# Kernel optimization log

Hardware: AMD Instinct MI355X
Metric: run time of the kernel (lower is better)

## Reference

```python
import jax, jax.numpy as jnp
import numpy as np

EPS_NN = 1e-8   # inverse-distance epsilon (PointNet++ three_interpolate)
EPS_BN = 1e-5   # BatchNorm eps


def three_nn_interpolate(points_coords, centers_coords, centers_features):
    # points_coords: [B,3,N], centers_coords: [B,3,M], centers_features: [B,C,M]
    # squared pairwise distances [B,N,M]
    d2 = jnp.sum((points_coords[:, :, :, None] - centers_coords[:, :, None, :]) ** 2, axis=1)
    neg_d, idx = jax.lax.top_k(-d2, 3)            # idx: [B,N,3]
    dist = -neg_d                                  # 3 smallest squared distances
    w = 1.0 / (dist + EPS_NN)
    w = w / jnp.sum(w, axis=-1, keepdims=True)     # [B,N,3]
    # gather center features at the 3 neighbors -> [B,C,N,3]
    f = jnp.take_along_axis(centers_features[:, :, None, :], idx[:, None, :, :], axis=3)
    return jnp.sum(f * w[:, None, :, :], axis=-1)  # [B,C,N]


def conv_bn_relu(x, w, b, gamma, beta):
    # x: [B,Cin,N], w: [Cout,Cin] (1x1 Conv1d), BatchNorm1d (training-mode batch stats)
    y = jnp.einsum('oc,bcn->bon', w, x) + b[None, :, None]
    mean = jnp.mean(y, axis=(0, 2), keepdims=True)
    var = jnp.var(y, axis=(0, 2), keepdims=True)
    y = (y - mean) * jax.lax.rsqrt(var + EPS_BN)
    y = y * gamma[None, :, None] + beta[None, :, None]
    return jax.nn.relu(y)


def setup_inputs() -> dict:
    key = jax.random.key(0)
    ks = jax.random.split(key, 10)
    B, N, M, C, C2 = 8, 8192, 2048, 256, 256
    Cin = C + C2
    O1, O2 = 256, 256
    return {
        'points_coords': jax.random.normal(ks[0], (B, 3, N), dtype=jnp.float32),
        'centers_coords': jax.random.normal(ks[1], (B, 3, M), dtype=jnp.float32),
        'centers_features': jax.random.normal(ks[2], (B, C, M), dtype=jnp.float32),
        'points_features': jax.random.normal(ks[3], (B, C2, N), dtype=jnp.float32),
        'w1': jax.random.normal(ks[4], (O1, Cin), dtype=jnp.float32) * (1.0 / np.sqrt(Cin)),
        'b1': jnp.zeros((O1,), dtype=jnp.float32),
        'gamma1': jnp.ones((O1,), dtype=jnp.float32),
        'beta1': jnp.zeros((O1,), dtype=jnp.float32),
        'w2': jax.random.normal(ks[5], (O2, O1), dtype=jnp.float32) * (1.0 / np.sqrt(O1)),
        'b2': jnp.zeros((O2,), dtype=jnp.float32),
        'gamma2': jnp.ones((O2,), dtype=jnp.float32),
        'beta2': jnp.zeros((O2,), dtype=jnp.float32),
    }


def reference(points_coords, centers_coords, centers_features, points_features,
              w1, b1, gamma1, beta1, w2, b2, gamma2, beta2):
    interp = three_nn_interpolate(points_coords, centers_coords, centers_features)  # [B,C,N]
    x = jnp.concatenate([interp, points_features], axis=1)                          # [B,C+C2,N]
    x = conv_bn_relu(x, w1, b1, gamma1, beta1)
    x = conv_bn_relu(x, w2, b2, gamma2, beta2)
    return (x, points_coords)
```

## Files before the change

kernel.cpp:

```cpp
#include <hip/hip_runtime.h>


#define BB 8
#define NN 8192
#define MM 2048
#define CF 256
#define CP 256

typedef float f4 __attribute__((ext_vector_type(4)));
typedef short s8v __attribute__((ext_vector_type(8)));

union U4 { uint4 u; s8v s; };

#define OFF_IDX    ((size_t)0)
#define OFF_WGT    ((size_t)1 << 20)
#define OFF_INTERP ((size_t)2 << 20)
#define OFF_P1S    (OFF_INTERP + (size_t)BB*CF*NN*4)
#define OFF_P1Q    (OFF_P1S + (size_t)512*256*4)
#define OFF_P2S    (OFF_P1Q + (size_t)512*256*4)
#define OFF_P2Q    (OFF_P2S + (size_t)512*256*4)
#define OFF_PAR1   (OFF_P2Q + (size_t)512*256*4)
#define OFF_PAR2   (OFF_PAR1 + (size_t)256*8)
#define OFF_WP1    (OFF_PAR2 + (size_t)256*8)
#define OFF_WP2    (OFF_WP1 + (size_t)524288)

__device__ __forceinline__ f4 relu4(f4 v) {
    v.x = fmaxf(v.x, 0.f); v.y = fmaxf(v.y, 0.f);
    v.z = fmaxf(v.z, 0.f); v.w = fmaxf(v.w, 0.f);
    return v;
}

__device__ __forceinline__ ushort bfrn(float x) {
    unsigned u = __float_as_uint(x);
    return (ushort)((u + 0x7FFFu + ((u >> 16) & 1u)) >> 16);
}
__device__ __forceinline__ void split1(float v, ushort& h, ushort& lo) {
    h = bfrn(v);
    float hf = __uint_as_float(((unsigned)h) << 16);
    lo = bfrn(v - hf);
}
__device__ __forceinline__ uint4 pack8(const ushort* h) {
    uint4 u;
    u.x = (unsigned)h[0] | ((unsigned)h[1] << 16);
    u.y = (unsigned)h[2] | ((unsigned)h[3] << 16);
    u.z = (unsigned)h[4] | ((unsigned)h[5] << 16);
    u.w = (unsigned)h[6] | ((unsigned)h[7] << 16);
    return u;
}

__global__ void k_wsplit(const float* __restrict__ w1, const float* __restrict__ w2,
                         uint4* __restrict__ wp1, uint4* __restrict__ wp2) {
    int i = blockIdx.x * 256 + threadIdx.x;
    const float* src; uint4* dst; int kt, o, kh, kdim;
    if (i < 16384) { kdim = 512; kt = i >> 10; int r = i & 1023; o = r >> 2; kh = r & 3; src = w1; dst = wp1; }
    else { int j = i - 16384; kdim = 256; kt = j >> 10; int r = j & 1023; o = r >> 2; kh = r & 3; src = w2; dst = wp2; }
    const float* p = src + o * kdim + kt * 32 + kh * 8;
    ushort hh[8], ll[8];
    #pragma unroll
    for (int k = 0; k < 8; ++k) split1(p[k], hh[k], ll[k]);
    uint4* slab = dst + kt * 2048 + o * 8;
    slab[kh ^ (o & 7)] = pack8(hh);
    slab[(kh + 4) ^ (o & 7)] = pack8(ll);
}

__device__ __forceinline__ void ins3(float d, int i,
                                     float& d0, int& i0, float& d1, int& i1,
                                     float& d2, int& i2) {
    const bool c0 = d < d0, c1 = d < d1, c2 = d < d2;
    i2 = c1 ? i1 : (c2 ? i : i2);
    i1 = c0 ? i0 : (c1 ? i : i1);
    i0 = c0 ? i  : i0;
    d2 = __builtin_amdgcn_fmed3f(d, d1, d2);
    d1 = __builtin_amdgcn_fmed3f(d, d0, d1);
    d0 = fminf(d, d0);
}

__global__ __launch_bounds__(256) void k_threenn(const float* __restrict__ pc,
                                                 const float* __restrict__ cen,
                                                 int* __restrict__ idx,
                                                 float* __restrict__ wgt) {
    __shared__ f4 c4[MM + 4];
    const int b  = blockIdx.x >> 7;
    const int n0 = (blockIdx.x & 127) << 6;
    const float* cb = cen + b * 3 * MM;
    for (int m = threadIdx.x; m < MM; m += 256) {
        f4 v = {cb[m], cb[MM + m], cb[2 * MM + m], 0.f};
        c4[m + (m >> 9)] = v;
    }
    __syncthreads();
    const int pt  = threadIdx.x >> 2;
    const int sub = threadIdx.x & 3;
    const int n = n0 + pt;
    const float* pb = pc + b * 3 * NN;
    const float px = pb[n], py = pb[NN + n], pz = pb[2 * NN + n];
    float d0 = 3e38f, d1 = 3e38f, d2 = 3e38f;
    int   i0 = 0,    i1 = 0,    i2 = 0;
    const f4* cbase = c4 + sub * 513;
    const int m0 = sub * 512;
    for (int mm = 0; mm < 512; mm += 8) {
        #pragma unroll
        for (int u = 0; u < 8; ++u) {
            f4 cm = cbase[mm + u];
            float dx = px - cm.x, dy = py - cm.y, dz = pz - cm.z;
            float d = fmaf(dz, dz, fmaf(dy, dy, dx * dx));
            ins3(d, m0 + mm + u, d0, i0, d1, i1, d2, i2);
        }
    }
    #pragma unroll
    for (int m = 1; m <= 2; m <<= 1) {
        float e0 = __shfl_xor(d0, m), e1 = __shfl_xor(d1, m), e2 = __shfl_xor(d2, m);
        int   j0 = __shfl_xor(i0, m), j1 = __shfl_xor(i1, m), j2 = __shfl_xor(i2, m);
        ins3(e0, j0, d0, i0, d1, i1, d2, i2);
        ins3(e1, j1, d0, i0, d1, i1, d2, i2);
        ins3(e2, j2, d0, i0, d1, i1, d2, i2);
    }
    if (sub == 0) {
        float w0 = 1.f / (d0 + 1e-8f), w1 = 1.f / (d1 + 1e-8f), w2 = 1.f / (d2 + 1e-8f);
        float inv = 1.f / (w0 + w1 + w2);
        const int p = b * NN + n;
        *(int4*)(idx + p * 4) = make_int4(i0, i1, i2, 0);
        f4 wv = {w0 * inv, w1 * inv, w2 * inv, 0.f};
        *(f4*)(wgt + p * 4) = wv;
    }
}

__global__ __launch_bounds__(512) void k_interp(const float* __restrict__ cf,
                                                const int* __restrict__ idx,
                                                const float* __restrict__ wgt,
                                                float* __restrict__ itp) {
    __shared__ float2 l2[4][MM];
    const int blk = blockIdx.x;
    const int b  = blk >> 6;
    const int cg = (blk >> 1) & 31;
    const int nh = blk & 1;
    const int tid = threadIdx.x;
    const float* cbase = cf + ((size_t)b * CF + cg * 8) * MM;
    #pragma unroll
    for (int q = 0; q < 4; ++q) {
        f4 ae = *(const f4*)(cbase + (2 * q) * MM + tid * 4);
        f4 ao = *(const f4*)(cbase + (2 * q + 1) * MM + tid * 4);
        #pragma unroll
        for (int i = 0; i < 4; ++i) l2[q][tid * 4 + i] = make_float2(ae[i], ao[i]);
    }
    __syncthreads();
    const int nb = nh * 4096;
    float* op = itp + ((size_t)b * CF + cg * 8) * NN + nb;
    #pragma unroll 2
    for (int it = 0; it < 8; ++it) {
        const int nn = it * 512 + tid;
        const int p = b * NN + nb + nn;
        const int4 iv = *(const int4*)(idx + p * 4);
        const f4   wv = *(const f4*)(wgt + p * 4);
        #pragma unroll
        for (int q = 0; q < 4; ++q) {
            float2 v0 = l2[q][iv.x], v1 = l2[q][iv.y], v2 = l2[q][iv.z];
            float sx = fmaf(v0.x, wv.x, fmaf(v1.x, wv.y, v2.x * wv.z));
            float sy = fmaf(v0.y, wv.x, fmaf(v1.y, wv.y, v2.y * wv.z));
            op[(size_t)(2 * q) * NN + nn]     = sx;
            op[(size_t)(2 * q + 1) * NN + nn] = sy;
        }
    }
}

template<int KDIM, bool BNIN>
__global__ __launch_bounds__(256, 2) void k_gemm(const float* xa,
                                                 const float* __restrict__ xb,
                                                 const uint4* __restrict__ wp,
                                                 float* yo,
                                                 const float2* __restrict__ par,
                                                 float* __restrict__ ps,
                                                 float* __restrict__ pq) {
    __shared__ __align__(16) unsigned char lds[49152];
    const int tid = threadIdx.x;
    const int b  = blockIdx.x >> 6;
    const int n0 = (blockIdx.x & 63) << 7;
    const int nl = tid & 127;
    const int kq = (tid >> 7) << 4;
    const int l = tid & 63, w = tid >> 6;
    const int lr = l & 15, lk = l >> 4;
    const int sw = (nl & 7) << 4;
    const int h0 = kq >> 3;

    f4 acc[4][8];
    #pragma unroll
    for (int mo = 0; mo < 4; ++mo)
        #pragma unroll
        for (int nn = 0; nn < 8; ++nn) acc[mo][nn] = (f4){0.f, 0.f, 0.f, 0.f};

    float xp[16];
    {
        const float* s = xa + ((size_t)b * 256 + kq) * NN + n0 + nl;
        #pragma unroll
        for (int i = 0; i < 16; ++i) xp[i] = s[i * NN];
    }

    for (int kt = 0; kt < KDIM / 32; ++kt) {
        const int c0 = kt * 32 + kq;
        __syncthreads();
        {
            ushort hh[16], ll[16];
            #pragma unroll
            for (int i = 0; i < 16; ++i) {
                float v = xp[i];
                if constexpr (BNIN) {
                    float2 pr = par[c0 + i];
                    v = fmaxf(fmaf(v, pr.x, pr.y), 0.f);
                }
                split1(v, hh[i], ll[i]);
            }
            const int xrow = nl << 7;
            *(uint4*)(lds + xrow + (((h0    ) << 4) ^ sw)) = pack8(hh);
            *(uint4*)(lds + xrow + (((h0 + 1) << 4) ^ sw)) = pack8(hh + 8);
            *(uint4*)(lds + xrow + (((h0 + 4) << 4) ^ sw)) = pack8(ll);
            *(uint4*)(lds + xrow + (((h0 + 5) << 4) ^ sw)) = pack8(ll + 8);
        }
        {
            const uint4* wsrc = wp + kt * 2048 + tid;
            #pragma unroll
            for (int c = 0; c < 8; ++c) {
                uint4 v = wsrc[c * 256];
                *(uint4*)(lds + 16384 + c * 4096 + tid * 16) = v;
            }
        }
        __syncthreads();
        if (kt + 1 < KDIM / 32) {
            const int c1 = (kt + 1) * 32 + kq;
            const float* s = (KDIM == 512 && c1 >= 256)
                ? xb + ((size_t)b * 256 + (c1 - 256)) * NN + n0 + nl
                : xa + ((size_t)b * 256 + c1) * NN + n0 + nl;
            #pragma unroll
            for (int i = 0; i < 16; ++i) xp[i] = s[i * NN];
        }
        U4 Ah[4], Al[4];
        #pragma unroll
        for (int mo = 0; mo < 4; ++mo) {
            const int o = w * 64 + mo * 16 + lr;
            const unsigned char* r = lds + 16384 + o * 128;
            const int osw = (o & 7) << 4;
            Ah[mo].u = *(const uint4*)(r + ((lk << 4) ^ osw));
            Al[mo].u = *(const uint4*)(r + ((64 + (lk << 4)) ^ osw));
        }
        #pragma unroll
        for (int nn = 0; nn < 8; ++nn) {
            const int n = nn * 16 + lr;
            const unsigned char* r = lds + n * 128;
            const int nsw = (n & 7) << 4;
            U4 Bh, Bl;
            Bh.u = *(const uint4*)(r + ((lk << 4) ^ nsw));
            Bl.u = *(const uint4*)(r + ((64 + (lk << 4)) ^ nsw));
            #pragma unroll
            for (int mo = 0; mo < 4; ++mo)
                acc[mo][nn] = __builtin_amdgcn_mfma_f32_16x16x32_bf16(Ah[mo].s, Bh.s, acc[mo][nn], 0, 0, 0);
            #pragma unroll
            for (int mo = 0; mo < 4; ++mo)
                acc[mo][nn] = __builtin_amdgcn_mfma_f32_16x16x32_bf16(Al[mo].s, Bh.s, acc[mo][nn], 0, 0, 0);
            #pragma unroll
            for (int mo = 0; mo < 4; ++mo)
                acc[mo][nn] = __builtin_amdgcn_mfma_f32_16x16x32_bf16(Ah[mo].s, Bl.s, acc[mo][nn], 0, 0, 0);
        }
    }

    float sv[4][4], qv[4][4];
    #pragma unroll
    for (int mo = 0; mo < 4; ++mo)
        #pragma unroll
        for (int j = 0; j < 4; ++j) { sv[mo][j] = 0.f; qv[mo][j] = 0.f; }
    #pragma unroll
    for (int mo = 0; mo < 4; ++mo)
        #pragma unroll
        for (int nn = 0; nn < 8; ++nn)
            #pragma unroll
            for (int j = 0; j < 4; ++j) {
                float a = acc[mo][nn][j];
                sv[mo][j] += a; qv[mo][j] += a * a;
            }
    #pragma unroll
    for (int m = 1; m < 16; m <<= 1)
        #pragma unroll
        for (int mo = 0; mo < 4; ++mo)
            #pragma unroll
            for (int j = 0; j < 4; ++j) {
                sv[mo][j] += __shfl_xor(sv[mo][j], m, 64);
                qv[mo][j] += __shfl_xor(qv[mo][j], m, 64);
            }
    if (lr == 0) {
        #pragma unroll
        for (int mo = 0; mo < 4; ++mo) {
            const int o0 = w * 64 + mo * 16 + lk * 4;
            f4 vs = {sv[mo][0], sv[mo][1], sv[mo][2], sv[mo][3]};
            f4 vq = {qv[mo][0], qv[mo][1], qv[mo][2], qv[mo][3]};
            *(f4*)(ps + blockIdx.x * 256 + o0) = vs;
            *(f4*)(pq + blockIdx.x * 256 + o0) = vq;
        }
    }
    float* yb = yo + (size_t)b * 256 * NN + n0;
    #pragma unroll
    for (int mo = 0; mo < 4; ++mo)
        #pragma unroll
        for (int j = 0; j < 4; ++j) {
            float* row = yb + (size_t)(w * 64 + mo * 16 + lk * 4 + j) * NN + lr;
            #pragma unroll
            for (int nn = 0; nn < 8; ++nn) row[nn * 16] = acc[mo][nn][j];
        }
}

__global__ void k_params(const float* __restrict__ ps, const float* __restrict__ pq,
                         const float* __restrict__ gamma, const float* __restrict__ beta,
                         float2* __restrict__ out) {
    __shared__ float rs[256], rq[256];
    const int oo = threadIdx.x & 15, seg = threadIdx.x >> 4;
    const int o = blockIdx.x * 16 + oo;
    float s = 0.f, q = 0.f;
    for (int blk = seg; blk < 512; blk += 16) {
        s += ps[blk * 256 + o];
        q += pq[blk * 256 + o];
    }
    rs[threadIdx.x] = s; rq[threadIdx.x] = q;
    __syncthreads();
    if (seg == 0) {
        float S = 0.f, Q = 0.f;
        #pragma unroll
        for (int g = 0; g < 16; ++g) { S += rs[g * 16 + oo]; Q += rq[g * 16 + oo]; }
        float mean = S * (1.f / 65536.f);
        float var  = Q * (1.f / 65536.f) - mean * mean;
        float rstd = rsqrtf(var + 1e-5f);
        float sc = gamma[o] * rstd;
        out[o] = make_float2(sc, beta[o] - mean * sc);
    }
}

__global__ __launch_bounds__(256) void k_final(float* __restrict__ yy,
                                               const float2* __restrict__ par) {
    int i = blockIdx.x * 256 + threadIdx.x;
    #pragma unroll 4
    for (int t = i; t < 4194304; t += 524288) {
        f4 v = ((f4*)yy)[t];
        float2 pr = par[(t >> 11) & 255];
        v = relu4(v * pr.x + pr.y);
        ((f4*)yy)[t] = v;
    }
}

extern "C" void kernel_launch(void* const* d_in, const int* in_sizes, int n_in,
                              void* d_out, int out_size, void* d_ws, size_t ws_size,
                              hipStream_t stream) {
    const float* pc  = (const float*)d_in[0];
    const float* cen = (const float*)d_in[1];
    const float* cf  = (const float*)d_in[2];
    const float* pf  = (const float*)d_in[3];
    const float* w1  = (const float*)d_in[4];
    const float* g1  = (const float*)d_in[6];
    const float* be1 = (const float*)d_in[7];
    const float* w2  = (const float*)d_in[8];
    const float* g2  = (const float*)d_in[10];
    const float* be2 = (const float*)d_in[11];

    char* ws = (char*)d_ws;
    int*    idx  = (int*)  (ws + OFF_IDX);
    float*  wgt  = (float*)(ws + OFF_WGT);
    float*  itp  = (float*)(ws + OFF_INTERP);
    float*  p1s  = (float*)(ws + OFF_P1S);
    float*  p1q  = (float*)(ws + OFF_P1Q);
    float*  p2s  = (float*)(ws + OFF_P2S);
    float*  p2q  = (float*)(ws + OFF_P2Q);
    float2* par1 = (float2*)(ws + OFF_PAR1);
    float2* par2 = (float2*)(ws + OFF_PAR2);
    uint4*  wp1  = (uint4*)(ws + OFF_WP1);
    uint4*  wp2  = (uint4*)(ws + OFF_WP2);
    float*  out  = (float*)d_out;

    k_wsplit<<<96, 256, 0, stream>>>(w1, w2, wp1, wp2);
    k_threenn<<<1024, 256, 0, stream>>>(pc, cen, idx, wgt);
    k_interp<<<512, 512, 0, stream>>>(cf, idx, wgt, itp);
    k_gemm<512, false><<<512, 256, 0, stream>>>(itp, pf, wp1, out, par1, p1s, p1q);
    k_params<<<16, 256, 0, stream>>>(p1s, p1q, g1, be1, par1);
    k_gemm<256, true><<<512, 256, 0, stream>>>(out, out, wp2, out, par1, p2s, p2q);
    k_params<<<16, 256, 0, stream>>>(p2s, p2q, g2, be2, par2);
    k_final<<<2048, 256, 0, stream>>>(out, par2);
    (void)hipMemcpyAsync(out + 16777216, pc, (size_t)BB * 3 * NN * 4,
                         hipMemcpyDeviceToDevice, stream);
}
```

Baseline: 231.3 us.

## Pack candidate index into distance low bits and use packed min/max top-6 filter

Each thread now handles two query points at once using packed float2 math, and runs the inner 3-NN loop on keys whose low 9 mantissa bits are replaced by the local center index. Insertion into a top-6 list is then pure packed min/max with no index tracking. A second exact pass recomputes full-precision distances for the 6 survivors and selects the true top 3. The aim is to cut per-candidate VALU work, which dominates the brute-force search, and to reuse each shared-memory center load across two points. Truncating the mantissa can misorder near-ties, so the 6-candidate buffer is relied on to keep the exact 3 nearest.

```diff
diff --git a/kernel.cpp b/kernel.cpp
--- a/kernel.cpp
+++ b/kernel.cpp
@@ -8,9 +8,12 @@
 #define CP 256
 
 typedef float f4 __attribute__((ext_vector_type(4)));
+typedef float f2 __attribute__((ext_vector_type(2)));
+typedef unsigned int u2 __attribute__((ext_vector_type(2)));
 typedef short s8v __attribute__((ext_vector_type(8)));
 
 union U4 { uint4 u; s8v s; };
+union UF2 { f2 f; u2 u; };
 
 #define OFF_IDX    ((size_t)0)
 #define OFF_WGT    ((size_t)1 << 20)
@@ -75,13 +78,21 @@
     d0 = fminf(d, d0);
 }
 
+__device__ __forceinline__ void inskey6(f2 kf, f2* k) {
+    #pragma unroll
+    for (int t = 5; t >= 1; --t)
+        k[t] = __builtin_elementwise_min(
+                   __builtin_elementwise_max(kf, k[t - 1]), k[t]);
+    k[0] = __builtin_elementwise_min(kf, k[0]);
+}
+
 __global__ __launch_bounds__(256) void k_threenn(const float* __restrict__ pc,
                                                  const float* __restrict__ cen,
                                                  int* __restrict__ idx,
                                                  float* __restrict__ wgt) {
     __shared__ f4 c4[MM + 4];
-    const int b  = blockIdx.x >> 7;
-    const int n0 = (blockIdx.x & 127) << 6;
+    const int b  = blockIdx.x >> 6;
+    const int n0 = (blockIdx.x & 63) << 7;
     const float* cb = cen + b * 3 * MM;
     for (int m = threadIdx.x; m < MM; m += 256) {
         f4 v = {cb[m], cb[MM + m], cb[2 * MM + m], 0.f};
@@ -90,37 +101,67 @@
     __syncthreads();
     const int pt  = threadIdx.x >> 2;
     const int sub = threadIdx.x & 3;
-    const int n = n0 + pt;
+    const int na = n0 + pt, nb = n0 + 64 + pt;
     const float* pb = pc + b * 3 * NN;
-    const float px = pb[n], py = pb[NN + n], pz = pb[2 * NN + n];
-    float d0 = 3e38f, d1 = 3e38f, d2 = 3e38f;
-    int   i0 = 0,    i1 = 0,    i2 = 0;
+    f2 pxp = {pb[na], pb[nb]};
+    f2 pyp = {pb[NN + na], pb[NN + nb]};
+    f2 pzp = {pb[2 * NN + na], pb[2 * NN + nb]};
+
+    f2 k6[6];
+    #pragma unroll
+    for (int t = 0; t < 6; ++t) k6[t] = (f2){3.3e38f, 3.3e38f};
     const f4* cbase = c4 + sub * 513;
-    const int m0 = sub * 512;
     for (int mm = 0; mm < 512; mm += 8) {
         #pragma unroll
         for (int u = 0; u < 8; ++u) {
             f4 cm = cbase[mm + u];
-            float dx = px - cm.x, dy = py - cm.y, dz = pz - cm.z;
+            f2 dx = pxp - cm.x, dy = pyp - cm.y, dz = pzp - cm.z;
+            f2 d = __builtin_elementwise_fma(dz, dz,
+                       __builtin_elementwise_fma(dy, dy, dx * dx));
+            UF2 uk; uk.f = d;
+            uk.u = (uk.u & 0xFFFFFE00u) | (unsigned)(mm + u);
+            inskey6(uk.f, k6);
+        }
+    }
+    const int m0 = sub * 512;
+    float d0[2], d1[2], d2[2]; int i0[2], i1[2], i2[2];
+    #pragma unroll
+    for (int j = 0; j < 2; ++j) {
+        d0[j] = 3e38f; d1[j] = 3e38f; d2[j] = 3e38f;
+        i0[j] = 0; i1[j] = 0; i2[j] = 0;
+        const float pxs = j ? pxp.y : pxp.x;
+        const float pys = j ? pyp.y : pyp.x;
+        const float pzs = j ? pzp.y : pzp.x;
+        #pragma unroll
+        for (int t = 0; t < 6; ++t) {
+            UF2 uk; uk.f = k6[t];
+            const int mg = m0 + (int)((j ? uk.u.y : uk.u.x) & 0x1FFu);
+            f4 cm = c4[mg + (mg >> 9)];
+            float dx = pxs - cm.x, dy = pys - cm.y, dz = pzs - cm.z;
             float d = fmaf(dz, dz, fmaf(dy, dy, dx * dx));
-            ins3(d, m0 + mm + u, d0, i0, d1, i1, d2, i2);
-        }
-    }
-    #pragma unroll
-    for (int m = 1; m <= 2; m <<= 1) {
-        float e0 = __shfl_xor(d0, m), e1 = __shfl_xor(d1, m), e2 = __shfl_xor(d2, m);
-        int   j0 = __shfl_xor(i0, m), j1 = __shfl_xor(i1, m), j2 = __shfl_xor(i2, m);
-        ins3(e0, j0, d0, i0, d1, i1, d2, i2);
-        ins3(e1, j1, d0, i0, d1, i1, d2, i2);
-        ins3(e2, j2, d0, i0, d1, i1, d2, i2);
-    }
+            ins3(d, mg, d0[j], i0[j], d1[j], i1[j], d2[j], i2[j]);
+        }
+    }
+    #pragma unroll
+    for (int m = 1; m <= 2; m <<= 1)
+        #pragma unroll
+        for (int j = 0; j < 2; ++j) {
+            float e0 = __shfl_xor(d0[j], m), e1 = __shfl_xor(d1[j], m), e2 = __shfl_xor(d2[j], m);
+            int   j0 = __shfl_xor(i0[j], m), j1 = __shfl_xor(i1[j], m), j2 = __shfl_xor(i2[j], m);
+            ins3(e0, j0, d0[j], i0[j], d1[j], i1[j], d2[j], i2[j]);
+            ins3(e1, j1, d0[j], i0[j], d1[j], i1[j], d2[j], i2[j]);
+            ins3(e2, j2, d0[j], i0[j], d1[j], i1[j], d2[j], i2[j]);
+        }
     if (sub == 0) {
-        float w0 = 1.f / (d0 + 1e-8f), w1 = 1.f / (d1 + 1e-8f), w2 = 1.f / (d2 + 1e-8f);
-        float inv = 1.f / (w0 + w1 + w2);
-        const int p = b * NN + n;
-        *(int4*)(idx + p * 4) = make_int4(i0, i1, i2, 0);
-        f4 wv = {w0 * inv, w1 * inv, w2 * inv, 0.f};
-        *(f4*)(wgt + p * 4) = wv;
+        #pragma unroll
+        for (int j = 0; j < 2; ++j) {
+            float w0 = 1.f / (d0[j] + 1e-8f), w1 = 1.f / (d1[j] + 1e-8f), w2 = 1.f / (d2[j] + 1e-8f);
+            float inv = 1.f / (w0 + w1 + w2);
+            const int p = b * NN + (j ? nb : na);
+            *(int4*)(idx + p * 4) = make_int4(i0[j], i1[j], i2[j], 0);
+            f4 wv = {w0 * inv, w1 * inv, w2 * inv, 0.f};
+            *(f4*)(wgt + p * 4) = wv;
+        }
     }
 }
 
@@ -370,7 +411,7 @@
     float*  out  = (float*)d_out;
 
     k_wsplit<<<96, 256, 0, stream>>>(w1, w2, wp1, wp2);
-    k_threenn<<<1024, 256, 0, stream>>>(pc, cen, idx, wgt);
+    k_threenn<<<512, 256, 0, stream>>>(pc, cen, idx, wgt);
     k_interp<<<512, 512, 0, stream>>>(cf, idx, wgt, itp);
     k_gemm<512, false><<<512, 256, 0, stream>>>(itp, pf, wp1, out, par1, p1s, p1q);
     k_params<<<16, 256, 0, stream>>>(p1s, p1q, g1, be1, par1);
```

New measurement: 237.1 us. +2.5%, slower.
